# Performance work log

Measured on AMD Instinct MI355X. Metric: run time of the kernel, lower is better.

The kernel has to match this reference:

```python
import math
import jax, jax.numpy as jnp
import numpy as np

N_HEAD = 16
BLOCK_SIZE = 2048


def setup_inputs() -> dict:
    key = jax.random.key(0)
    ks = jax.random.split(key, 6)
    B, L, D = 2, 2048, 1024
    hs = D // N_HEAD
    s = 0.02
    return {
        "x": jax.random.normal(ks[0], (B, L, D), dtype=jnp.float32),
        "Wqkv": jax.random.normal(ks[1], (D, 3 * D), dtype=jnp.float32) * s,
        "bqkv": jax.random.normal(ks[2], (3 * D,), dtype=jnp.float32) * s,
        "Wproj": jax.random.normal(ks[3], (D, D), dtype=jnp.float32) * s,
        "bproj": jax.random.normal(ks[4], (D,), dtype=jnp.float32) * s,
        "Er": jax.random.normal(ks[5], (BLOCK_SIZE, hs), dtype=jnp.float32),
    }


def _skew(QEr):
    # QEr: [B, H, L, L] -> pad one zero column on the left, reshape, drop first row
    B, H, R, C = QEr.shape
    padded = jnp.pad(QEr, ((0, 0), (0, 0), (0, 0), (1, 0)))  # [B,H,R,C+1]
    reshaped = padded.reshape(B, H, C + 1, R)
    return reshaped[:, :, 1:, :]  # [B,H,R,C]


def reference(x, Wqkv, bqkv, Wproj, bproj, Er):
    B, L, D = x.shape
    H = N_HEAD
    hs = D // H
    qkv = x @ Wqkv + bqkv  # [B,L,3D]
    q, k, v = jnp.split(qkv, 3, axis=-1)
    q = q.reshape(B, L, H, hs).transpose(0, 2, 1, 3)  # [B,H,L,hs]
    k = k.reshape(B, L, H, hs).transpose(0, 2, 1, 3)
    v = v.reshape(B, L, H, hs).transpose(0, 2, 1, 3)

    Er_used = Er[BLOCK_SIZE - L:, :]           # [L, hs]
    QEr = jnp.einsum('bhld,md->bhlm', q, Er_used)  # q @ Er^T -> [B,H,L,L]
    Srel = _skew(QEr)

    scale = 1.0 / math.sqrt(hs)
    att = (jnp.einsum('bhld,bhmd->bhlm', q, k) + Srel) * scale
    causal = jnp.tril(jnp.ones((L, L), dtype=bool))
    att = jnp.where(causal[None, None], att, -jnp.inf)
    att = jax.nn.softmax(att, axis=-1)
    y = jnp.einsum('bhlm,bhmd->bhld', att, v)  # [B,H,L,hs]
    y = y.transpose(0, 2, 1, 3).reshape(B, L, D)
    return y @ Wproj + bproj
```

## Files before the change

kernel.cpp:

```cpp
#include <hip/hip_runtime.h>
#include <hip/hip_bf16.h>

#define LSEQ 2048
#define NH 16
#define HS 64
#define DIM 1024

typedef __attribute__((ext_vector_type(8))) short short8;
typedef __attribute__((ext_vector_type(4))) float f32x4;

typedef const __attribute__((address_space(1))) void g_void_t;
typedef __attribute__((address_space(3))) void s_void_t;

#define QSCALE 0.18033688011112042f

static __device__ __forceinline__ short f2bf(float f) {
  __hip_bfloat16 h = __float2bfloat16(f);
  return __builtin_bit_cast(short, h);
}

static __device__ __forceinline__ float fexp2(float x) {
#if __has_builtin(__builtin_amdgcn_exp2f)
  return __builtin_amdgcn_exp2f(x);
#else
  float r; asm("v_exp_f32 %0, %1" : "=v"(r) : "v"(x)); return r;
#endif
}

template<int CTRL>
static __device__ __forceinline__ float dpp_mov(float x) {
  return __builtin_bit_cast(float,
      __builtin_amdgcn_update_dpp(0, __builtin_bit_cast(int, x), CTRL, 0xF, 0xF, true));
}
static __device__ __forceinline__ float redmax16(float x) {
  x = fmaxf(x, dpp_mov<0xB1>(x));
  x = fmaxf(x, dpp_mov<0x4E>(x));
  x = fmaxf(x, dpp_mov<0x141>(x));
  x = fmaxf(x, dpp_mov<0x140>(x));
  return x;
}
static __device__ __forceinline__ float redsum16(float x) {
  x += dpp_mov<0xB1>(x);
  x += dpp_mov<0x4E>(x);
  x += dpp_mov<0x141>(x);
  x += dpp_mov<0x140>(x);
  return x;
}


__global__ void prep_kernel(const float* __restrict__ x, const float* __restrict__ Er,
                            const float* __restrict__ Wqkv, const float* __restrict__ Wproj,
                            short* __restrict__ xb, short* __restrict__ Erb,
                            short* __restrict__ WqkvT, short* __restrict__ WprojT) {
  __shared__ float tile[64][65];
  int bid = blockIdx.x;
  if (bid < 4224) {
    const float* in; short* out; int i0;
    if (bid < 4096) { in = x;  out = xb;  i0 = bid * 256; }
    else            { in = Er; out = Erb; i0 = (bid - 4096) * 256; }
    int i = i0 + threadIdx.x;
    float4 v = reinterpret_cast<const float4*>(in)[i];
    short4 o;
    o.x = f2bf(v.x); o.y = f2bf(v.y); o.z = f2bf(v.z); o.w = f2bf(v.w);
    reinterpret_cast<short4*>(out)[i] = o;
    return;
  }
  int id = bid - 4224;
  const float* W; short* Wt; int N, tx, ty;
  if (id < 768) { W = Wqkv;  Wt = WqkvT;  N = 3072; tx = id % 48; ty = id / 48; }
  else { id -= 768; W = Wproj; Wt = WprojT; N = 1024; tx = id % 16; ty = id / 16; }
  const int K = 1024;
  int k0 = ty * 64, n0 = tx * 64;
  int t = threadIdx.x;
  int r4 = t >> 6, cc = t & 63;
  for (int i = 0; i < 16; ++i) {
    int row = i * 4 + r4;
    tile[row][cc] = W[(size_t)(k0 + row) * N + (n0 + cc)];
  }
  __syncthreads();
  for (int i = 0; i < 16; ++i) {
    int row = i * 4 + r4;
    Wt[(size_t)(n0 + row) * K + (k0 + cc)] = f2bf(tile[cc][row]);
  }
}

__global__ void transpose_v_kernel(const short* __restrict__ V, short* __restrict__ Vt) {
  __shared__ short tile[64][65];
  int bh = blockIdx.y;
  int l0 = blockIdx.x * 64;
  int t = threadIdx.x;
  const short* src = V + ((size_t)bh * LSEQ + l0) * HS;
  for (int i = 0; i < 2; ++i) {
    int ch = i * 256 + t;
    int row = ch >> 3, c8 = ch & 7;
    uint4 v = *reinterpret_cast<const uint4*>(src + row * HS + c8 * 8);
    short tmp[8];
    *reinterpret_cast<uint4*>(tmp) = v;
#pragma unroll
    for (int e = 0; e < 8; ++e) tile[row][c8 * 8 + e] = tmp[e];
  }
  __syncthreads();
  short* dst = Vt + (size_t)bh * HS * LSEQ + l0;
  for (int i = 0; i < 2; ++i) {
    int ch = i * 256 + t;
    int d = ch >> 3, c8 = ch & 7;
    short tmp[8];
#pragma unroll
    for (int e = 0; e < 8; ++e) tmp[e] = tile[c8 * 8 + e][d];
    *reinterpret_cast<uint4*>(dst + (size_t)d * LSEQ + c8 * 8) = *reinterpret_cast<uint4*>(tmp);
  }
}


template<int MODE>
__global__ __launch_bounds__(256, 2) void gemm_bt_kernel(
    const short* __restrict__ A, const short* __restrict__ Bt,
    const float* __restrict__ bias, int M, int N, int K,
    short* __restrict__ oq, short* __restrict__ ok, short* __restrict__ ov,
    float* __restrict__ of)
{
  __shared__ short Al[128 * 32];
  __shared__ short Bl[128 * 32];
  const int m0 = blockIdx.y * 128, n0 = blockIdx.x * 128;
  const int t = threadIdx.x;
  const int lane = t & 63, wave = t >> 6;
  const int wr = wave >> 1, wc = wave & 1;
  const int g = lane >> 4, c = lane & 15;
  f32x4 acc[4][4] = {};

  for (int k0 = 0; k0 < K; k0 += 32) {
    __syncthreads();
    for (int i = 0; i < 2; ++i) {
      int ch = i * 256 + t;
      int row = ch >> 2, c8 = ch & 3;
      __builtin_amdgcn_global_load_lds(
          (g_void_t*)(A + (size_t)(m0 + row) * K + k0 + c8 * 8),
          (s_void_t*)(Al + (i * 256 + wave * 64) * 8), 16, 0, 0);
      __builtin_amdgcn_global_load_lds(
          (g_void_t*)(Bt + (size_t)(n0 + row) * K + k0 + c8 * 8),
          (s_void_t*)(Bl + (i * 256 + wave * 64) * 8), 16, 0, 0);
    }
    __syncthreads();
    short8 af[4], bf[4];
#pragma unroll
    for (int mi = 0; mi < 4; ++mi) {
      int row = wr * 64 + mi * 16 + c;
      af[mi] = *reinterpret_cast<const short8*>(Al + row * 32 + g * 8);
    }
#pragma unroll
    for (int ni = 0; ni < 4; ++ni) {
      int row = wc * 64 + ni * 16 + c;
      bf[ni] = *reinterpret_cast<const short8*>(Bl + row * 32 + g * 8);
    }
#pragma unroll
    for (int mi = 0; mi < 4; ++mi)
#pragma unroll
      for (int ni = 0; ni < 4; ++ni)
        acc[mi][ni] = __builtin_amdgcn_mfma_f32_16x16x32_bf16(af[mi], bf[ni], acc[mi][ni], 0, 0, 0);
  }

#pragma unroll
  for (int mi = 0; mi < 4; ++mi)
#pragma unroll
    for (int ni = 0; ni < 4; ++ni) {
      int n = n0 + wc * 64 + ni * 16 + c;
      float bv = bias[n];
#pragma unroll
      for (int r = 0; r < 4; ++r) {
        int m = m0 + wr * 64 + mi * 16 + g * 4 + r;
        float val = acc[mi][ni][r] + bv;
        if (MODE == 0) {
          int which = n >> 10;
          int hh2 = (n >> 6) & 15;
          int d = n & 63;
          int b = m >> 11, ll = m & 2047;
          if (which == 0) val *= QSCALE;
          short* dst = which == 0 ? oq : (which == 1 ? ok : ov);
          dst[(((size_t)b * NH + hh2) * LSEQ + ll) * HS + d] = f2bf(val);
        } else {
          of[(size_t)m * N + n] = val;
        }
      }
    }
}


__global__ __launch_bounds__(256, 2) void attn_kernel(
    const short* __restrict__ Qb, const short* __restrict__ Kb,
    const short* __restrict__ VTb, const short* __restrict__ Erb,
    short* __restrict__ Y)
{
  const int bid = blockIdx.x;
  const int p = 15 - (bid >> 5);
  const int bh = bid & 31;
  const int qtH = 2 * p + 1, qtL = 2 * p;
  const int l0H = qtH * 64, l0L = qtL * 64;
  const int nbase = 30 - 2 * p;
  const int bb = bh >> 4, hh = bh & 15;
  const int t = threadIdx.x;
  const int lane = t & 63, wave = t >> 6;
  const int g = lane >> 4, c = lane & 15;
  const int r8 = lane >> 3;
  const int c16b = (lane & 7) * 16;

  __shared__ short Kl[64 * 64];
  __shared__ short Vl[2][64 * 64];
  __shared__ short El[4][64 * 64];
  __shared__ short Pl[4][16 * 64];

  const short* QgH = Qb + ((size_t)bh * LSEQ + l0H) * HS;
  const short* QgL = Qb + ((size_t)bh * LSEQ + l0L) * HS;
  short8 qfH[2], qfL[2];
#pragma unroll
  for (int kk = 0; kk < 2; ++kk) {
    qfH[kk] = *reinterpret_cast<const short8*>(QgH + (wave * 16 + c) * HS + kk * 32 + g * 8);
    qfL[kk] = *reinterpret_cast<const short8*>(QgL + (wave * 16 + c) * HS + kk * 32 + g * 8);
  }

  auto stage_K = [&](int step) {
    const char* Kg = (const char*)(Kb + ((size_t)bh * LSEQ + step * 64) * HS);
#pragma unroll
    for (int j = 0; j < 2; ++j) {
      int row = wave * 16 + j * 8 + r8;
      __builtin_amdgcn_global_load_lds(
          (g_void_t*)(Kg + row * 128 + (c16b ^ ((row & 7) << 4))),
          (s_void_t*)(&Kl[(wave * 16 + j * 8) * 64]), 16, 0, 0);
    }
  };
  auto stage_V = [&](int step) {
    int sel = step & 1;
#pragma unroll
    for (int j = 0; j < 2; ++j) {
      int row = wave * 16 + j * 8 + r8;
      const char* Vg = (const char*)(VTb + ((size_t)bh * HS + row) * LSEQ + step * 64);
      __builtin_amdgcn_global_load_lds(
          (g_void_t*)(Vg + (c16b ^ ((row & 7) << 4))),
          (s_void_t*)(&Vl[sel][(wave * 16 + j * 8) * 64]), 16, 0, 0);
    }
  };
  auto stage_E = [&](int chunk) {
    int slot = chunk & 3;
#pragma unroll
    for (int j = 0; j < 2; ++j) {
      int row = wave * 16 + j * 8 + r8;
      int e = chunk * 64 + row;
      if (e > LSEQ - 1) e = LSEQ - 1;
      __builtin_amdgcn_global_load_lds(
          (g_void_t*)((const char*)Erb + (size_t)e * 128 + (c16b ^ ((row & 7) << 4))),
          (s_void_t*)(&El[slot][(wave * 16 + j * 8) * 64]), 16, 0, 0);
    }
  };

  auto gs = [&](const short8* qf, int nT, f32x4* ga, f32x4* sa) {
#pragma unroll
    for (int s5 = 0; s5 < 5; ++s5) {
      int nsb = (3 - wave) + s5;
      int rb = nsb * 16 + c;
      int ch = nT + (rb >> 6);
      int phys = ((ch & 3) << 6) | (rb & 63);
      ga[s5] = (f32x4){0.0f, 0.0f, 0.0f, 0.0f};
#pragma unroll
      for (int kk = 0; kk < 2; ++kk) {
        int byte = phys * 128 + (((kk * 32 + g * 8) * 2) ^ ((rb & 7) << 4));
        short8 ef = *reinterpret_cast<const short8*>((char*)El + byte);
        ga[s5] = __builtin_amdgcn_mfma_f32_16x16x32_bf16(qf[kk], ef, ga[s5], 0, 0, 0);
      }
    }
#pragma unroll
    for (int ns = 0; ns < 4; ++ns) {
      sa[ns] = (f32x4){0.0f, 0.0f, 0.0f, 0.0f};
#pragma unroll
      for (int kk = 0; kk < 2; ++kk) {
        int row = ns * 16 + c;
        int byte = row * 128 + (((kk * 32 + g * 8) * 2) ^ ((row & 7) << 4));
        short8 kf = *reinterpret_cast<const short8*>((char*)Kl + byte);
        sa[ns] = __builtin_amdgcn_mfma_f32_16x16x32_bf16(qf[kk], kf, sa[ns], 0, 0, 0);
      }
    }
  };

  auto post = [&](f32x4* ga, f32x4* sa, bool diag, int selV,
                  f32x4* acc_o, float* mrun, float* lrun) {
    float sv[4][4];
#pragma unroll
    for (int r = 0; r < 4; ++r) {
      int i4 = g * 4 + r;
      int u0 = c + 15 - i4;
      int srcl = (g << 4) | (u0 & 15);
      float bp[5];
#pragma unroll
      for (int s5 = 0; s5 < 5; ++s5) bp[s5] = __shfl(ga[s5][r], srcl, 64);
      bool lo = (u0 < 16);
#pragma unroll
      for (int ns = 0; ns < 4; ++ns) {
        float srel = lo ? bp[ns] : bp[ns + 1];
        float xx = sa[ns][r] + srel;
        if (diag && (ns * 16 + c > wave * 16 + i4)) xx = -1e30f;
        sv[ns][r] = xx;
      }
    }

    float mx[4];
    bool need = false;
#pragma unroll
    for (int r = 0; r < 4; ++r) {
      float m = fmaxf(fmaxf(sv[0][r], sv[1][r]), fmaxf(sv[2][r], sv[3][r]));
      mx[r] = redmax16(m);
      need = need || (mx[r] > mrun[r] + 4.0f);
    }
    if (__ballot(need)) {
#pragma unroll
      for (int r = 0; r < 4; ++r) {
        float mnew = fmaxf(mrun[r], mx[r]);
        float al = fexp2(mrun[r] - mnew);
        mrun[r] = mnew;
        lrun[r] *= al;
#pragma unroll
        for (int ns = 0; ns < 4; ++ns) acc_o[ns][r] *= al;
      }
    }
#pragma unroll
    for (int ns = 0; ns < 4; ++ns)
#pragma unroll
      for (int r = 0; r < 4; ++r)
        sv[ns][r] = fexp2(sv[ns][r] - mrun[r]);
#pragma unroll
    for (int r = 0; r < 4; ++r) {
      float s = (sv[0][r] + sv[1][r]) + (sv[2][r] + sv[3][r]);
      lrun[r] += redsum16(s);
    }

    short* Pw = Pl[wave];
#pragma unroll
    for (int ns = 0; ns < 4; ++ns)
#pragma unroll
      for (int r = 0; r < 4; ++r) {
        int row = g * 4 + r;
        int byte = row * 128 + (((ns * 16 + c) * 2) ^ ((row & 7) << 4));
        *reinterpret_cast<short*>(reinterpret_cast<char*>(Pw) + byte) = f2bf(sv[ns][r]);
      }
#pragma unroll
    for (int kk = 0; kk < 2; ++kk) {
      int kbyte = (kk * 32 + g * 8) * 2;
      int byteP = c * 128 + (kbyte ^ ((c & 7) << 4));
      short8 pf = *reinterpret_cast<const short8*>(reinterpret_cast<char*>(Pw) + byteP);
#pragma unroll
      for (int ns = 0; ns < 4; ++ns) {
        int rowV = ns * 16 + c;
        int byteV = rowV * 128 + (kbyte ^ ((rowV & 7) << 4));
        short8 vf = *reinterpret_cast<const short8*>((char*)Vl[selV] + byteV);
        acc_o[ns] = __builtin_amdgcn_mfma_f32_16x16x32_bf16(pf, vf, acc_o[ns], 0, 0, 0);
      }
    }
  };

  stage_V(0);
  stage_K(0);
  stage_E(nbase); stage_E(nbase + 1); stage_E(nbase + 2);

  f32x4 accH[4] = {}, accL[4] = {};
  float mH[4], lH[4], mL[4], lL[4];
#pragma unroll
  for (int r = 0; r < 4; ++r) { mH[r] = -1e30f; lH[r] = 0.0f; mL[r] = -1e30f; lL[r] = 0.0f; }

  for (int s = 0; s <= qtH; ++s) {
    const int sel = s & 1;
    const bool doL = (s <= qtL);
    const int nH = nbase + s;

    asm volatile("s_waitcnt vmcnt(0)" ::: "memory");
    __builtin_amdgcn_s_barrier();
    __builtin_amdgcn_sched_barrier(0);

    f32x4 gaH[5], saH[4], gaL[5], saL[4];
    gs(qfH, nH, gaH, saH);
    if (doL) gs(qfL, nH + 1, gaL, saL);

    __builtin_amdgcn_sched_barrier(0);
    __builtin_amdgcn_s_barrier();
    __builtin_amdgcn_sched_barrier(0);

    if (s < qtH) {
      stage_V(s + 1);
      stage_K(s + 1);
      stage_E(nbase + s + 3);
    }

    post(gaH, saH, s == qtH, sel, accH, mH, lH);
    if (doL) post(gaL, saL, s == qtL, sel, accL, mL, lL);
  }

#pragma unroll
  for (int ns = 0; ns < 4; ++ns)
#pragma unroll
    for (int r = 0; r < 4; ++r) {
      int row = g * 4 + r;
      int d = ns * 16 + c;
      int lgH = l0H + wave * 16 + row;
      Y[((size_t)bb * LSEQ + lgH) * DIM + hh * HS + d] = f2bf(accH[ns][r] / lH[r]);
      int lgL = l0L + wave * 16 + row;
      Y[((size_t)bb * LSEQ + lgL) * DIM + hh * HS + d] = f2bf(accL[ns][r] / lL[r]);
    }
}


extern "C" void kernel_launch(void* const* d_in, const int* in_sizes, int n_in,
                              void* d_out, int out_size, void* d_ws, size_t ws_size,
                              hipStream_t stream)
{
  const float* x     = (const float*)d_in[0];
  const float* Wqkv  = (const float*)d_in[1];
  const float* bqkv  = (const float*)d_in[2];
  const float* Wproj = (const float*)d_in[3];
  const float* bproj = (const float*)d_in[4];
  const float* Er    = (const float*)d_in[5];

  char* ws = (char*)d_ws;
  short* xb     = (short*)(ws + 0);
  short* WqkvT  = (short*)(ws + 8388608);
  short* WprojT = (short*)(ws + 14680064);
  short* Erb    = (short*)(ws + 16777216);
  short* qB     = (short*)(ws + 17039360);
  short* kB     = (short*)(ws + 25427968);
  short* vB     = (short*)(ws + 33816576);
  short* yB     = (short*)(ws + 42205184);
  short* vT     = xb;

  prep_kernel<<<dim3(5248), 256, 0, stream>>>(x, Er, Wqkv, Wproj, xb, Erb, WqkvT, WprojT);

  gemm_bt_kernel<0><<<dim3(3072 / 128, 4096 / 128), 256, 0, stream>>>(
      xb, WqkvT, bqkv, 4096, 3072, 1024, qB, kB, vB, nullptr);

  transpose_v_kernel<<<dim3(32, 32), 256, 0, stream>>>(vB, vT);

  attn_kernel<<<dim3(512), 256, 0, stream>>>(qB, kB, vT, Erb, yB);

  gemm_bt_kernel<1><<<dim3(1024 / 128, 4096 / 128), 256, 0, stream>>>(
      yB, WprojT, bproj, 4096, 1024, 1024, nullptr, nullptr, nullptr, (float*)d_out);
}
```

Baseline: 170.1 us.

## Split attention blocks to one query tile each, load Er directly to registers

The attention kernel now gives each block a single 64-row query tile instead of a paired high/low tile, doubling the grid to 1024 blocks and raising the occupancy hint to 3 blocks per CU. The Er staging ring in LDS is removed; each wave loads its Er rows straight from global memory into registers every step, and K is double-buffered alongside V, which drops one barrier per iteration. This reduces LDS use and per-block register state so more blocks can be resident. The cost is losing the Q-tile pairing that shared K/V staging between two tiles, plus uncoalesced global Er reads inside the loop.

```diff
diff --git a/kernel.cpp b/kernel.cpp
--- a/kernel.cpp
+++ b/kernel.cpp
@@ -185,17 +185,15 @@
 }
 
 
-__global__ __launch_bounds__(256, 2) void attn_kernel(
+__global__ __launch_bounds__(256, 3) void attn_kernel(
     const short* __restrict__ Qb, const short* __restrict__ Kb,
     const short* __restrict__ VTb, const short* __restrict__ Erb,
     short* __restrict__ Y)
 {
   const int bid = blockIdx.x;
-  const int p = 15 - (bid >> 5);
+  const int qt = 31 - (bid >> 5);
   const int bh = bid & 31;
-  const int qtH = 2 * p + 1, qtL = 2 * p;
-  const int l0H = qtH * 64, l0L = qtL * 64;
-  const int nbase = 30 - 2 * p;
+  const int l0 = qt * 64;
   const int bb = bh >> 4, hh = bh & 15;
   const int t = threadIdx.x;
   const int lane = t & 63, wave = t >> 6;
@@ -203,32 +201,25 @@
   const int r8 = lane >> 3;
   const int c16b = (lane & 7) * 16;
 
-  __shared__ short Kl[64 * 64];
+  __shared__ short Kl[2][64 * 64];
   __shared__ short Vl[2][64 * 64];
-  __shared__ short El[4][64 * 64];
   __shared__ short Pl[4][16 * 64];
 
-  const short* QgH = Qb + ((size_t)bh * LSEQ + l0H) * HS;
-  const short* QgL = Qb + ((size_t)bh * LSEQ + l0L) * HS;
-  short8 qfH[2], qfL[2];
-#pragma unroll
-  for (int kk = 0; kk < 2; ++kk) {
-    qfH[kk] = *reinterpret_cast<const short8*>(QgH + (wave * 16 + c) * HS + kk * 32 + g * 8);
-    qfL[kk] = *reinterpret_cast<const short8*>(QgL + (wave * 16 + c) * HS + kk * 32 + g * 8);
-  }
-
-  auto stage_K = [&](int step) {
+  const short* Qg = Qb + ((size_t)bh * LSEQ + l0) * HS;
+  short8 qf[2];
+#pragma unroll
+  for (int kk = 0; kk < 2; ++kk)
+    qf[kk] = *reinterpret_cast<const short8*>(Qg + (wave * 16 + c) * HS + kk * 32 + g * 8);
+
+  auto stage = [&](int step, int sel) {
     const char* Kg = (const char*)(Kb + ((size_t)bh * LSEQ + step * 64) * HS);
 #pragma unroll
     for (int j = 0; j < 2; ++j) {
       int row = wave * 16 + j * 8 + r8;
       __builtin_amdgcn_global_load_lds(
           (g_void_t*)(Kg + row * 128 + (c16b ^ ((row & 7) << 4))),
-          (s_void_t*)(&Kl[(wave * 16 + j * 8) * 64]), 16, 0, 0);
-    }
-  };
-  auto stage_V = [&](int step) {
-    int sel = step & 1;
+          (s_void_t*)(&Kl[sel][(wave * 16 + j * 8) * 64]), 16, 0, 0);
+    }
 #pragma unroll
     for (int j = 0; j < 2; ++j) {
       int row = wave * 16 + j * 8 + r8;
@@ -238,34 +229,46 @@
           (s_void_t*)(&Vl[sel][(wave * 16 + j * 8) * 64]), 16, 0, 0);
     }
   };
-  auto stage_E = [&](int chunk) {
-    int slot = chunk & 3;
-#pragma unroll
-    for (int j = 0; j < 2; ++j) {
-      int row = wave * 16 + j * 8 + r8;
-      int e = chunk * 64 + row;
-      if (e > LSEQ - 1) e = LSEQ - 1;
-      __builtin_amdgcn_global_load_lds(
-          (g_void_t*)((const char*)Erb + (size_t)e * 128 + (c16b ^ ((row & 7) << 4))),
-          (s_void_t*)(&El[slot][(wave * 16 + j * 8) * 64]), 16, 0, 0);
-    }
-  };
-
-  auto gs = [&](const short8* qf, int nT, f32x4* ga, f32x4* sa) {
+
+  stage(0, 0);
+
+  f32x4 acc_o[4] = {};
+  float mrun[4], lrun[4];
+#pragma unroll
+  for (int r = 0; r < 4; ++r) { mrun[r] = -1e30f; lrun[r] = 0.0f; }
+
+  for (int s = 0; s <= qt; ++s) {
+    const int sel = s & 1;
+    const bool diag = (s == qt);
+
+    asm volatile("s_waitcnt vmcnt(0)" ::: "memory");
+    __builtin_amdgcn_s_barrier();
+    __builtin_amdgcn_sched_barrier(0);
+
+    short8 er[5][2];
+    {
+      int ebase = 1984 + 64 * (s - qt) + (3 - wave) * 16 + c;
+#pragma unroll
+      for (int s5 = 0; s5 < 5; ++s5) {
+        int e = ebase + s5 * 16;
+        if (e > LSEQ - 1) e = LSEQ - 1;
+        const short* ep = Erb + (size_t)e * HS + g * 8;
+        er[s5][0] = *reinterpret_cast<const short8*>(ep);
+        er[s5][1] = *reinterpret_cast<const short8*>(ep + 32);
+      }
+    }
+
+    if (s < qt) stage(s + 1, sel ^ 1);
+
+    f32x4 ga[5];
 #pragma unroll
     for (int s5 = 0; s5 < 5; ++s5) {
-      int nsb = (3 - wave) + s5;
-      int rb = nsb * 16 + c;
-      int ch = nT + (rb >> 6);
-      int phys = ((ch & 3) << 6) | (rb & 63);
       ga[s5] = (f32x4){0.0f, 0.0f, 0.0f, 0.0f};
-#pragma unroll
-      for (int kk = 0; kk < 2; ++kk) {
-        int byte = phys * 128 + (((kk * 32 + g * 8) * 2) ^ ((rb & 7) << 4));
-        short8 ef = *reinterpret_cast<const short8*>((char*)El + byte);
-        ga[s5] = __builtin_amdgcn_mfma_f32_16x16x32_bf16(qf[kk], ef, ga[s5], 0, 0, 0);
-      }
-    }
+      ga[s5] = __builtin_amdgcn_mfma_f32_16x16x32_bf16(qf[0], er[s5][0], ga[s5], 0, 0, 0);
+      ga[s5] = __builtin_amdgcn_mfma_f32_16x16x32_bf16(qf[1], er[s5][1], ga[s5], 0, 0, 0);
+    }
+
+    f32x4 sa[4];
 #pragma unroll
     for (int ns = 0; ns < 4; ++ns) {
       sa[ns] = (f32x4){0.0f, 0.0f, 0.0f, 0.0f};
@@ -273,14 +276,11 @@
       for (int kk = 0; kk < 2; ++kk) {
         int row = ns * 16 + c;
         int byte = row * 128 + (((kk * 32 + g * 8) * 2) ^ ((row & 7) << 4));
-        short8 kf = *reinterpret_cast<const short8*>((char*)Kl + byte);
+        short8 kf = *reinterpret_cast<const short8*>((char*)Kl[sel] + byte);
         sa[ns] = __builtin_amdgcn_mfma_f32_16x16x32_bf16(qf[kk], kf, sa[ns], 0, 0, 0);
       }
     }
-  };
-
-  auto post = [&](f32x4* ga, f32x4* sa, bool diag, int selV,
-                  f32x4* acc_o, float* mrun, float* lrun) {
+
     float sv[4][4];
 #pragma unroll
     for (int r = 0; r < 4; ++r) {
@@ -326,8 +326,8 @@
         sv[ns][r] = fexp2(sv[ns][r] - mrun[r]);
 #pragma unroll
     for (int r = 0; r < 4; ++r) {
-      float s = (sv[0][r] + sv[1][r]) + (sv[2][r] + sv[3][r]);
-      lrun[r] += redsum16(s);
+      float s2 = (sv[0][r] + sv[1][r]) + (sv[2][r] + sv[3][r]);
+      lrun[r] += redsum16(s2);
     }
 
     short* Pw = Pl[wave];
@@ -339,6 +339,7 @@
         int byte = row * 128 + (((ns * 16 + c) * 2) ^ ((row & 7) << 4));
         *reinterpret_cast<short*>(reinterpret_cast<char*>(Pw) + byte) = f2bf(sv[ns][r]);
       }
+
 #pragma unroll
     for (int kk = 0; kk < 2; ++kk) {
       int kbyte = (kk * 32 + g * 8) * 2;
@@ -348,46 +349,10 @@
       for (int ns = 0; ns < 4; ++ns) {
         int rowV = ns * 16 + c;
         int byteV = rowV * 128 + (kbyte ^ ((rowV & 7) << 4));
-        short8 vf = *reinterpret_cast<const short8*>((char*)Vl[selV] + byteV);
+        short8 vf = *reinterpret_cast<const short8*>((char*)Vl[sel] + byteV);
         acc_o[ns] = __builtin_amdgcn_mfma_f32_16x16x32_bf16(pf, vf, acc_o[ns], 0, 0, 0);
       }
     }
-  };
-
-  stage_V(0);
-  stage_K(0);
-  stage_E(nbase); stage_E(nbase + 1); stage_E(nbase + 2);
-
-  f32x4 accH[4] = {}, accL[4] = {};
-  float mH[4], lH[4], mL[4], lL[4];
-#pragma unroll
-  for (int r = 0; r < 4; ++r) { mH[r] = -1e30f; lH[r] = 0.0f; mL[r] = -1e30f; lL[r] = 0.0f; }
-
-  for (int s = 0; s <= qtH; ++s) {
-    const int sel = s & 1;
-    const bool doL = (s <= qtL);
-    const int nH = nbase + s;
-
-    asm volatile("s_waitcnt vmcnt(0)" ::: "memory");
-    __builtin_amdgcn_s_barrier();
-    __builtin_amdgcn_sched_barrier(0);
-
-    f32x4 gaH[5], saH[4], gaL[5], saL[4];
-    gs(qfH, nH, gaH, saH);
-    if (doL) gs(qfL, nH + 1, gaL, saL);
-
-    __builtin_amdgcn_sched_barrier(0);
-    __builtin_amdgcn_s_barrier();
-    __builtin_amdgcn_sched_barrier(0);
-
-    if (s < qtH) {
-      stage_V(s + 1);
-      stage_K(s + 1);
-      stage_E(nbase + s + 3);
-    }
-
-    post(gaH, saH, s == qtH, sel, accH, mH, lH);
-    if (doL) post(gaL, saL, s == qtL, sel, accL, mL, lL);
   }
 
 #pragma unroll
@@ -395,11 +360,9 @@
 #pragma unroll
     for (int r = 0; r < 4; ++r) {
       int row = g * 4 + r;
+      int lg = l0 + wave * 16 + row;
       int d = ns * 16 + c;
-      int lgH = l0H + wave * 16 + row;
-      Y[((size_t)bb * LSEQ + lgH) * DIM + hh * HS + d] = f2bf(accH[ns][r] / lH[r]);
-      int lgL = l0L + wave * 16 + row;
-      Y[((size_t)bb * LSEQ + lgL) * DIM + hh * HS + d] = f2bf(accL[ns][r] / lL[r]);
+      Y[((size_t)bb * LSEQ + lg) * DIM + hh * HS + d] = f2bf(acc_o[ns][r] / lrun[r]);
     }
 }
 
@@ -433,7 +396,7 @@
 
   transpose_v_kernel<<<dim3(32, 32), 256, 0, stream>>>(vB, vT);
 
-  attn_kernel<<<dim3(512), 256, 0, stream>>>(qB, kB, vT, Erb, yB);
+  attn_kernel<<<dim3(1024), 256, 0, stream>>>(qB, kB, vT, Erb, yB);
 
   gemm_bt_kernel<1><<<dim3(1024 / 128, 4096 / 128), 256, 0, stream>>>(
       yB, WprojT, bproj, 4096, 1024, 1024, nullptr, nullptr, nullptr, (float*)d_out);
```

Result: slower. 229.7 us (+35.0%).
